# Kernel tuning notes

Measured on AMD Instinct MI355X. Metric: run time of the kernel, lower is better.

The kernel has to match this reference:

```python
import jax, jax.numpy as jnp
import numpy as np

N = 20000   # num_nodes
D = 128     # node_dim
H = 128     # hidden_dim (also per-head channels, PyG out_channels is per-head)
EV = 64     # event_dim
NH = 4      # heads
E = 250000  # num edges
NT = 8      # num_event_types
K = 4       # active event types


def setup_inputs() -> dict:
    key = jax.random.key(0)
    ks = jax.random.split(key, 24)
    def w(i, shape, s=0.05):
        return jax.random.normal(ks[i], shape, dtype=jnp.float32) * s
    z = lambda shape: jnp.zeros(shape, jnp.float32)
    o = lambda shape: jnp.ones(shape, jnp.float32)
    return {
        "node_ids": jnp.arange(N, dtype=jnp.int32),
        "event_type_ids": jax.random.randint(ks[0], (K,), 0, NT, dtype=jnp.int32),
        "src": jax.random.randint(ks[1], (E,), 0, N, dtype=jnp.int32),
        "dst": jax.random.randint(ks[2], (E,), 0, N, dtype=jnp.int32),
        "event_features": jax.random.normal(ks[3], (EV,), dtype=jnp.float32),
        "event_intensity": jax.random.uniform(ks[4], (K,), dtype=jnp.float32),
        "node_emb_table": w(5, (N, D), 1.0),
        "event_type_table": w(6, (NT, H), 0.5),
        "ev_w1": w(7, (EV, H)), "ev_b1": z((H,)), "ev_g1": o((H,)), "ev_bt1": z((H,)),
        "ev_w2": w(8, (H, H)), "ev_b2": z((H,)), "ev_g2": o((H,)), "ev_bt2": z((H,)),
        "wq": w(9, (D + H, NH * H)), "bq": z((NH * H,)),
        "wk": w(10, (D + H, NH * H)), "bk": z((NH * H,)),
        "wv": w(11, (D + H, NH * H)), "bv": z((NH * H,)),
        "wskip": w(12, (D + H, H)), "bskip": z((H,)),
        "g0_w": w(13, (H, NH * H)), "g0_as": w(14, (NH, H), 0.1), "g0_ad": w(15, (NH, H), 0.1), "g0_b": z((H,)),
        "g1_w": w(16, (H, NH * H)), "g1_as": w(17, (NH, H), 0.1), "g1_ad": w(18, (NH, H), 0.1), "g1_b": z((H,)),
        "wih": w(19, (H, 4 * H)), "whh": w(20, (H, 4 * H)), "bih": z((4 * H,)), "bhh": z((4 * H,)),
    }


def layer_norm(x, g, b, eps=1e-5):
    mu = jnp.mean(x, axis=-1, keepdims=True)
    var = jnp.mean(jnp.square(x - mu), axis=-1, keepdims=True)
    return (x - mu) * jax.lax.rsqrt(var + eps) * g + b


def segment_softmax(logits, seg, n):
    # logits: [E, NH]; softmax over edges sharing the same destination seg id
    m = jax.ops.segment_max(logits, seg, num_segments=n)
    m = jnp.where(jnp.isfinite(m), m, 0.0)  # guard empty segments
    e = jnp.exp(logits - m[seg])
    s = jax.ops.segment_sum(e, seg, num_segments=n)
    return e / (s[seg] + 1e-16)


def _forward(node_ids, event_type_ids, src, dst,
             event_features, event_intensity, node_emb_table, event_type_table,
             ev_w1, ev_b1, ev_g1, ev_bt1, ev_w2, ev_b2, ev_g2, ev_bt2,
             wq, bq, wk, bk, wv, bv, wskip, bskip,
             g0_w, g0_as, g0_ad, g0_b, g1_w, g1_as, g1_ad, g1_b,
             wih, whh, bih, bhh):
    node_emb = node_emb_table[node_ids]                                      # [N, D]
    # event encoder MLP (dropout off / eval mode)
    e = jax.nn.relu(layer_norm(event_features @ ev_w1 + ev_b1, ev_g1, ev_bt1))
    e = jax.nn.relu(layer_norm(e @ ev_w2 + ev_b2, ev_g2, ev_bt2))            # [H]
    # intensity-weighted mean of active event-type embeddings
    e = e + jnp.mean(event_type_table[event_type_ids] * event_intensity[:, None], axis=0)
    x = jnp.concatenate([node_emb, jnp.broadcast_to(e, (N, H))], axis=1)     # [N, D+H]

    # --- TransformerConv (heads=NH, concat=False -> head mean, root_weight skip) ---
    q = (x @ wq + bq).reshape(N, NH, H)
    k = (x @ wk + bk).reshape(N, NH, H)
    v = (x @ wv + bv).reshape(N, NH, H)
    alpha = jnp.sum(q[dst] * k[src], axis=-1) / jnp.sqrt(jnp.float32(H))     # [E, NH]
    alpha = segment_softmax(alpha, dst, N)
    agg = jax.ops.segment_sum(v[src] * alpha[..., None], dst, num_segments=N)  # [N, NH, H]
    x = agg.mean(axis=1) + x @ wskip + bskip                                 # [N, H]

    sl = jnp.arange(N, dtype=src.dtype)
    src2 = jnp.concatenate([src, sl])
    dst2 = jnp.concatenate([dst, sl])
    for w_, asrc, adst, b_ in ((g0_w, g0_as, g0_ad, g0_b), (g1_w, g1_as, g1_ad, g1_b)):
        xh = (x @ w_).reshape(N, NH, H)
        a_s = jnp.sum(xh * asrc, axis=-1)                                    # [N, NH]
        a_d = jnp.sum(xh * adst, axis=-1)
        ee = jax.nn.leaky_relu(a_s[src2] + a_d[dst2], 0.2)                   # [E+N, NH]
        a = segment_softmax(ee, dst2, N)
        out = jax.ops.segment_sum(xh[src2] * a[..., None], dst2, num_segments=N)
        x = jax.nn.relu(out.mean(axis=1) + b_)                               # [N, H]

    # --- batched LSTMCell, zero initial (h, c); torch gate order i, f, g, o ---
    h0 = jnp.zeros((N, H), x.dtype)
    c0 = jnp.zeros((N, H), x.dtype)
    gates = x @ wih + bih + h0 @ whh + bhh                                   # [N, 4H]
    gi, gf, gg, go = jnp.split(gates, 4, axis=-1)
    c = jax.nn.sigmoid(gf) * c0 + jax.nn.sigmoid(gi) * jnp.tanh(gg)
    h = jax.nn.sigmoid(go) * jnp.tanh(c)
    return h, c


def reference(node_ids, event_type_ids, src, dst,
              event_features, event_intensity, node_emb_table, event_type_table,
              ev_w1, ev_b1, ev_g1, ev_bt1, ev_w2, ev_b2, ev_g2, ev_bt2,
              wq, bq, wk, bk, wv, bv, wskip, bskip,
              g0_w, g0_as, g0_ad, g0_b, g1_w, g1_as, g1_ad, g1_b,
              wih, whh, bih, bhh):
    return _forward(node_ids, event_type_ids, src, dst,
                    event_features, event_intensity, node_emb_table, event_type_table,
                    ev_w1, ev_b1, ev_g1, ev_bt1, ev_w2, ev_b2, ev_g2, ev_bt2,
                    wq, bq, wk, bk, wv, bv, wskip, bskip,
                    g0_w, g0_as, g0_ad, g0_b, g1_w, g1_as, g1_ad, g1_b,
                    wih, whh, bih, bhh)
```

## Files before the change

### kernel.cpp

```cpp
#include <hip/hip_runtime.h>
#include <math.h>

#define D_DIM 128
#define H_DIM 128
#define SQRT_H_INV 0.08838834764831845f
#define BCOL_QKV 0
#define BCOL_G0 1664
#define BCOL_G1 2176
#define BCOL_W  2688
#define BCOL_TOT 3072

typedef unsigned short u16;
typedef unsigned short ushort8v __attribute__((ext_vector_type(8)));
typedef __bf16 bf16x8 __attribute__((ext_vector_type(8)));
typedef float f32x4 __attribute__((ext_vector_type(4)));


__device__ __forceinline__ float grp16_sum(float v) {
  v += __shfl_xor(v, 1);
  v += __shfl_xor(v, 2);
  v += __shfl_xor(v, 4);
  v += __shfl_xor(v, 8);
  return v;
}

__device__ __forceinline__ void split_bf16(float x, u16& h, u16& l) {
  __bf16 hb = (__bf16)x;
  float rm = x - (float)hb;
  __bf16 lb = (__bf16)rm;
  h = __builtin_bit_cast(u16, hb);
  l = __builtin_bit_cast(u16, lb);
}

__global__ __launch_bounds__(128) void k_event(
    const float* __restrict__ ef, int EV,
    const float* __restrict__ w1, const float* __restrict__ b1,
    const float* __restrict__ g1, const float* __restrict__ bt1,
    const float* __restrict__ w2, const float* __restrict__ b2,
    const float* __restrict__ g2, const float* __restrict__ bt2,
    const float* __restrict__ ett, const int* __restrict__ etid,
    const float* __restrict__ inten, int K,
    float* __restrict__ e_out)
{
  __shared__ float sh[H_DIM];
  __shared__ float red[H_DIM];
  const int t = threadIdx.x;

  float acc = b1[t];
  for (int i = 0; i < EV; ++i) acc += ef[i] * w1[i * H_DIM + t];

  red[t] = acc; __syncthreads();
  for (int s = 64; s > 0; s >>= 1) { if (t < s) red[t] += red[t + s]; __syncthreads(); }
  float mu = red[0] / H_DIM; __syncthreads();
  float d = acc - mu;
  red[t] = d * d; __syncthreads();
  for (int s = 64; s > 0; s >>= 1) { if (t < s) red[t] += red[t + s]; __syncthreads(); }
  float var = red[0] / H_DIM; __syncthreads();
  float y = d * rsqrtf(var + 1e-5f) * g1[t] + bt1[t];
  y = fmaxf(y, 0.f);
  sh[t] = y; __syncthreads();

  float acc2 = b2[t];
  for (int i = 0; i < H_DIM; ++i) acc2 += sh[i] * w2[i * H_DIM + t];

  red[t] = acc2; __syncthreads();
  for (int s = 64; s > 0; s >>= 1) { if (t < s) red[t] += red[t + s]; __syncthreads(); }
  mu = red[0] / H_DIM; __syncthreads();
  d = acc2 - mu;
  red[t] = d * d; __syncthreads();
  for (int s = 64; s > 0; s >>= 1) { if (t < s) red[t] += red[t + s]; __syncthreads(); }
  var = red[0] / H_DIM; __syncthreads();
  float y2 = d * rsqrtf(var + 1e-5f) * g2[t] + bt2[t];
  y2 = fmaxf(y2, 0.f);

  float m = 0.f;
  for (int k = 0; k < K; ++k) m += ett[etid[k] * H_DIM + t] * inten[k];
  e_out[t] = y2 + m / (float)K;
}

__global__ __launch_bounds__(256) void k_cvec_all(
    const float* __restrict__ e,
    const float* __restrict__ wq, const float* __restrict__ bq,
    const float* __restrict__ wk, const float* __restrict__ bk,
    const float* __restrict__ wv, const float* __restrict__ bv,
    const float* __restrict__ wskip, const float* __restrict__ bskip,
    const float* __restrict__ bih, const float* __restrict__ bhh,
    float* __restrict__ cvec1, float* __restrict__ cvec2)
{
  __shared__ float es[H_DIM];
  const int t = threadIdx.x;
  if (t < H_DIM) es[t] = e[t];
  __syncthreads();
  int j = blockIdx.x * 256 + t;
  if (j < 1664) {
    const float* W; const float* b; int col; int stride;
    if (j < 512)       { W = wq;    b = bq;    col = j;        stride = 512; }
    else if (j < 1024) { W = wk;    b = bk;    col = j - 512;  stride = 512; }
    else if (j < 1536) { W = wv;    b = bv;    col = j - 1024; stride = 512; }
    else               { W = wskip; b = bskip; col = j - 1536; stride = 128; }
    float a = b[col];
    for (int i = 0; i < H_DIM; ++i) a += es[i] * W[(D_DIM + i) * stride + col];
    cvec1[j] = a;
  } else if (j < 1664 + 384) {
    int j2 = j - 1664;
    int src = (j2 < 128) ? j2 : j2 + 128;
    cvec2[j2] = bih[src] + bhh[src];
  }
}

__global__ __launch_bounds__(256) void k_split_all(
    const float* __restrict__ wq, const float* __restrict__ wk,
    const float* __restrict__ wv, const float* __restrict__ wskip,
    const float* __restrict__ g0w, const float* __restrict__ g1w,
    const float* __restrict__ wih,
    u16* __restrict__ hi, u16* __restrict__ lo)
{
  int idx = blockIdx.x * 256 + threadIdx.x;
  if (idx >= BCOL_TOT * 16) return;
  int n = idx >> 4, g = idx & 15;
  const float* W; int col, stride;
  if (n < 512)        { W = wq;    col = n;        stride = 512; }
  else if (n < 1024)  { W = wk;    col = n - 512;  stride = 512; }
  else if (n < 1536)  { W = wv;    col = n - 1024; stride = 512; }
  else if (n < 1664)  { W = wskip; col = n - 1536; stride = 128; }
  else if (n < 2176)  { W = g0w;   col = n - 1664; stride = 512; }
  else if (n < 2688)  { W = g1w;   col = n - 2176; stride = 512; }
  else { int c = n - 2688; W = wih; col = (c < 128) ? c : c + 128; stride = 512; }
  size_t dst = (size_t)(n >> 4) * 2048 + g * 128 + (n & 15) * 8;
#pragma unroll
  for (int j = 0; j < 8; ++j) {
    u16 h, l;
    split_bf16(W[(size_t)(g * 8 + j) * stride + col], h, l);
    hi[dst + j] = h; lo[dst + j] = l;
  }
}

__global__ __launch_bounds__(256) void k_split_a(
    const float* __restrict__ A, const int* __restrict__ ids,
    u16* __restrict__ hi, u16* __restrict__ lo, int M, int Mpad)
{
  int idx = blockIdx.x * 256 + threadIdx.x;
  if (idx >= Mpad * 16) return;
  int row = idx >> 4, g = idx & 15;
  size_t dst = (size_t)(row >> 4) * 2048 + g * 128 + (row & 15) * 8;
  if (row < M) {
    int ar = ids ? ids[row] : row;
    const float* srcp = A + (size_t)ar * 128 + g * 8;
#pragma unroll
    for (int j = 0; j < 8; ++j) {
      u16 h, l;
      split_bf16(srcp[j], h, l);
      hi[dst + j] = h; lo[dst + j] = l;
    }
  } else {
#pragma unroll
    for (int j = 0; j < 8; ++j) { hi[dst + j] = 0; lo[dst + j] = 0; }
  }
}

__global__ __launch_bounds__(256, 3) void mfma_gemm(
    const u16* __restrict__ Ahi, const u16* __restrict__ Alo,
    const u16* __restrict__ Bhi, const u16* __restrict__ Blo,
    const float* __restrict__ cvec,
    u16* __restrict__ bf_out, int bf_cols,
    float* __restrict__ f32_out, int f32_lo, int ld_f32,
    const float* __restrict__ asw, const float* __restrict__ adw,
    float* __restrict__ a_s, float* __restrict__ a_d,
    int M)
{
  __shared__ float red[256];

  const int t = threadIdx.x;
  const int bm = blockIdx.y * 128;
  const int bn = blockIdx.x * 128;
  const int lane = t & 63;
  const int wid = t >> 6;
  const int wr = wid >> 1, wc = wid & 1;
  const int lg = lane >> 4;
  const int lr = lane & 15;

  const int arb = (bm >> 4) + wr * 4;
  const int brb = (bn >> 4) + wc * 4;

  f32x4 acc[4][4];
  const f32x4 zero = {0.f, 0.f, 0.f, 0.f};
#pragma unroll
  for (int i = 0; i < 4; ++i)
#pragma unroll
    for (int j = 0; j < 4; ++j) acc[i][j] = zero;

#pragma unroll
  for (int ks = 0; ks < 4; ++ks) {
    const int g = ks * 4 + lg;
    bf16x8 ah[4], al[4], bh[4], bl[4];
#pragma unroll
    for (int i = 0; i < 4; ++i) {
      size_t oa = (size_t)(arb + i) * 2048 + g * 128 + lr * 8;
      ah[i] = *(const bf16x8*)&Ahi[oa];
      al[i] = *(const bf16x8*)&Alo[oa];
      size_t ob = (size_t)(brb + i) * 2048 + g * 128 + lr * 8;
      bh[i] = *(const bf16x8*)&Bhi[ob];
      bl[i] = *(const bf16x8*)&Blo[ob];
    }
#pragma unroll
    for (int i = 0; i < 4; ++i)
#pragma unroll
      for (int j = 0; j < 4; ++j) {
        acc[i][j] = __builtin_amdgcn_mfma_f32_16x16x32_bf16(ah[i], bh[j], acc[i][j], 0, 0, 0);
        acc[i][j] = __builtin_amdgcn_mfma_f32_16x16x32_bf16(ah[i], bl[j], acc[i][j], 0, 0, 0);
        acc[i][j] = __builtin_amdgcn_mfma_f32_16x16x32_bf16(al[i], bh[j], acc[i][j], 0, 0, 0);
      }
  }

  const int rq = (lane >> 4) << 2;
  const int cq = lane & 15;
  const int head = bn >> 7;

  float ws_[4], wd_[4];
  if (asw) {
#pragma unroll
    for (int j = 0; j < 4; ++j) {
      int cc = (wc * 64 + j * 16 + cq) & 127;
      ws_[j] = asw[head * 128 + cc];
      wd_[j] = adw[head * 128 + cc];
    }
    if (t < 256) red[t] = 0.f;
    __syncthreads();
  }

#pragma unroll
  for (int i = 0; i < 4; ++i) {
#pragma unroll
    for (int r = 0; r < 4; ++r) {
      int rowl = wr * 64 + i * 16 + rq + r;
      int row = bm + rowl;
      bool rok = row < M;
      float ps = 0.f, pd = 0.f;
#pragma unroll
      for (int j = 0; j < 4; ++j) {
        int col = bn + wc * 64 + j * 16 + cq;
        float a = acc[i][j][r];
        if (rok) {
          float val = a + (cvec ? cvec[col] : 0.f);
          if (bf_out && col < bf_cols)
            bf_out[(size_t)row * bf_cols + col] =
                __builtin_bit_cast(u16, (__bf16)val);
          if (f32_out && col >= f32_lo)
            f32_out[(size_t)row * ld_f32 + (col - f32_lo)] = val;
        }
        if (asw) { ps += a * ws_[j]; pd += a * wd_[j]; }
      }
      if (asw && rok) {
        atomicAdd(&red[rowl], ps);
        atomicAdd(&red[128 + rowl], pd);
      }
    }
  }
  if (asw) {
    __syncthreads();
    if (t < 128) {
      int row = bm + t;
      if (row < M) {
        a_s[row * 4 + head] = red[t];
        a_d[row * 4 + head] = red[128 + t];
      }
    }
  }
}

__global__ __launch_bounds__(256) void k_zero(int* __restrict__ p, int n) {
  int i = blockIdx.x * 256 + threadIdx.x;
  if (i < n) p[i] = 0;
}
__global__ __launch_bounds__(256) void k_count(
    const int* __restrict__ dst, int* __restrict__ counts, int E) {
  int e = blockIdx.x * 256 + threadIdx.x;
  if (e < E) atomicAdd(&counts[dst[e]], 1);
}
__global__ __launch_bounds__(1024) void k_scan(
    const int* __restrict__ counts, int* __restrict__ offs,
    int* __restrict__ cursor, int N)
{
  __shared__ int wsum[16];
  const int t = threadIdx.x;
  const int lane = t & 63;
  const int wid = t >> 6;
  int running = 0;
  for (int base = 0; base < N; base += 1024) {
    int v = (base + t < N) ? counts[base + t] : 0;
    int incl = v;
#pragma unroll
    for (int s = 1; s < 64; s <<= 1) {
      int u = __shfl_up(incl, s);
      if (lane >= s) incl += u;
    }
    if (lane == 63) wsum[wid] = incl;
    __syncthreads();
    if (wid == 0) {
      int w = (lane < 16) ? wsum[lane] : 0;
#pragma unroll
      for (int s = 1; s < 16; s <<= 1) {
        int u = __shfl_up(w, s);
        if (lane >= s) w += u;
      }
      if (lane < 16) wsum[lane] = w;
    }
    __syncthreads();
    int wpre = (wid > 0) ? wsum[wid - 1] : 0;
    int tot = wsum[15];
    int inclg = incl + wpre;
    if (base + t < N) {
      offs[base + t + 1] = running + inclg;
      cursor[base + t] = running + inclg - v;
    }
    running += tot;
    __syncthreads();
  }
  if (t == 0) offs[0] = 0;
}
__global__ __launch_bounds__(256) void k_fill(
    const int* __restrict__ src, const int* __restrict__ dst,
    int* __restrict__ cursor, int* __restrict__ csr_src, int E) {
  int e = blockIdx.x * 256 + threadIdx.x;
  if (e < E) {
    int slot = atomicAdd(&cursor[dst[e]], 1);
    csr_src[slot] = src[e];
  }
}

__global__ __launch_bounds__(256) void k_tconv(
    const u16* __restrict__ QKVp, const float* __restrict__ skipbuf,
    const int* __restrict__ offs, const int* __restrict__ csr_src,
    u16* __restrict__ Xhi, u16* __restrict__ Xlo, int N)
{
  const int wid = threadIdx.x >> 6;
  const int lane = threadIdx.x & 63;
  const int node = blockIdx.x * 4 + wid;
  if (node >= N) {
    if (lane < 16) {
      size_t dst = (size_t)(node >> 4) * 2048 + lane * 128 + (node & 15) * 8;
#pragma unroll
      for (int j = 0; j < 8; ++j) { Xhi[dst + j] = 0; Xlo[dst + j] = 0; }
    }
    return;
  }
  float q[8];
  {
    bf16x8 qv = *(const bf16x8*)(QKVp + (size_t)node * 1536 + lane * 8);
#pragma unroll
    for (int j = 0; j < 8; ++j) q[j] = (float)qv[j];
  }
  const int beg = offs[node], end = offs[node + 1];
  float mx = -1e30f;
  float ssum = 0.f;
  float acc[8] = {0.f,0.f,0.f,0.f,0.f,0.f,0.f,0.f};

  int e = beg;
  for (; e + 4 <= end; e += 4) {
    int s0 = csr_src[e];
    int s1 = csr_src[e + 1];
    int s2 = csr_src[e + 2];
    int s3 = csr_src[e + 3];
    const u16* r0 = QKVp + (size_t)s0 * 1536 + 512 + lane * 8;
    const u16* r1 = QKVp + (size_t)s1 * 1536 + 512 + lane * 8;
    const u16* r2 = QKVp + (size_t)s2 * 1536 + 512 + lane * 8;
    const u16* r3 = QKVp + (size_t)s3 * 1536 + 512 + lane * 8;
    bf16x8 k0 = *(const bf16x8*)(r0);
    bf16x8 k1 = *(const bf16x8*)(r1);
    bf16x8 k2 = *(const bf16x8*)(r2);
    bf16x8 k3 = *(const bf16x8*)(r3);
    bf16x8 v0 = *(const bf16x8*)(r0 + 512);
    bf16x8 v1 = *(const bf16x8*)(r1 + 512);
    bf16x8 v2 = *(const bf16x8*)(r2 + 512);
    bf16x8 v3 = *(const bf16x8*)(r3 + 512);
    float p0 = 0.f, p1 = 0.f, p2 = 0.f, p3 = 0.f;
#pragma unroll
    for (int j = 0; j < 8; ++j) {
      p0 += q[j] * (float)k0[j];
      p1 += q[j] * (float)k1[j];
      p2 += q[j] * (float)k2[j];
      p3 += q[j] * (float)k3[j];
    }
    p0 = grp16_sum(p0) * SQRT_H_INV;
    p1 = grp16_sum(p1) * SQRT_H_INV;
    p2 = grp16_sum(p2) * SQRT_H_INV;
    p3 = grp16_sum(p3) * SQRT_H_INV;
    float nm = fmaxf(fmaxf(fmaxf(p0, p1), fmaxf(p2, p3)), mx);
    float sc = expf(mx - nm);
    float w0 = expf(p0 - nm);
    float w1 = expf(p1 - nm);
    float w2 = expf(p2 - nm);
    float w3 = expf(p3 - nm);
    ssum = ssum * sc + (w0 + w1) + (w2 + w3);
#pragma unroll
    for (int j = 0; j < 8; ++j)
      acc[j] = acc[j] * sc + (w0 * (float)v0[j] + w1 * (float)v1[j])
                           + (w2 * (float)v2[j] + w3 * (float)v3[j]);
    mx = nm;
  }
  for (; e < end; ++e) {
    int s0 = csr_src[e];
    const u16* r0 = QKVp + (size_t)s0 * 1536 + 512 + lane * 8;
    bf16x8 ka = *(const bf16x8*)(r0);
    bf16x8 va = *(const bf16x8*)(r0 + 512);
    float p0 = 0.f;
#pragma unroll
    for (int j = 0; j < 8; ++j) p0 += q[j] * (float)ka[j];
    p0 = grp16_sum(p0) * SQRT_H_INV;
    float nm = fmaxf(mx, p0);
    float sc = expf(mx - nm);
    float w0 = expf(p0 - nm);
    ssum = ssum * sc + w0;
#pragma unroll
    for (int j = 0; j < 8; ++j)
      acc[j] = acc[j] * sc + w0 * (float)va[j];
    mx = nm;
  }

  float inv = 1.f / (ssum + 1e-16f);
#pragma unroll
  for (int j = 0; j < 8; ++j) acc[j] *= inv;
#pragma unroll
  for (int j = 0; j < 8; ++j) {
    acc[j] += __shfl_xor(acc[j], 16);
    acc[j] += __shfl_xor(acc[j], 32);
  }
  if (lane < 16) {
    const float* sk = skipbuf + (size_t)node * 128 + lane * 8;
    size_t dst = (size_t)(node >> 4) * 2048 + lane * 128 + (node & 15) * 8;
#pragma unroll
    for (int j = 0; j < 8; ++j) {
      float x = 0.25f * acc[j] + sk[j];
      u16 h, l;
      split_bf16(x, h, l);
      Xhi[dst + j] = h; Xlo[dst + j] = l;
    }
  }
}

__global__ __launch_bounds__(256) void k_gat_agg(
    const u16* __restrict__ xhb,
    const float* __restrict__ a_s, const float* __restrict__ a_d,
    const int* __restrict__ offs, const int* __restrict__ csr_src,
    const float* __restrict__ bias,
    u16* __restrict__ Xhi, u16* __restrict__ Xlo, int N)
{
  const int wid = threadIdx.x >> 6;
  const int lane = threadIdx.x & 63;
  const int node = blockIdx.x * 4 + wid;
  if (node >= N) {
    if (lane < 16) {
      size_t dst = (size_t)(node >> 4) * 2048 + lane * 128 + (node & 15) * 8;
#pragma unroll
      for (int j = 0; j < 8; ++j) { Xhi[dst + j] = 0; Xlo[dst + j] = 0; }
    }
    return;
  }
  const int head = lane >> 4;
  const float adn = a_d[node * 4 + head];
  const float asn = a_s[node * 4 + head];
  float lself = asn + adn;
  lself = lself >= 0.f ? lself : 0.2f * lself;

  float mx = lself;
  float ssum = 1.f;
  float acc[8];
  {
    bf16x8 xs = *(const bf16x8*)(xhb + (size_t)node * 512 + lane * 8);
#pragma unroll
    for (int j = 0; j < 8; ++j) acc[j] = (float)xs[j];
  }

  const int beg = offs[node], end = offs[node + 1];
  int e = beg;
  for (; e + 4 <= end; e += 4) {
    int s0 = csr_src[e];
    int s1 = csr_src[e + 1];
    int s2 = csr_src[e + 2];
    int s3 = csr_src[e + 3];
    float l0 = a_s[s0 * 4 + head];
    float l1 = a_s[s1 * 4 + head];
    float l2 = a_s[s2 * 4 + head];
    float l3 = a_s[s3 * 4 + head];
    const u16* r0 = xhb + (size_t)s0 * 512 + lane * 8;
    const u16* r1 = xhb + (size_t)s1 * 512 + lane * 8;
    const u16* r2 = xhb + (size_t)s2 * 512 + lane * 8;
    const u16* r3 = xhb + (size_t)s3 * 512 + lane * 8;
    bf16x8 xa = *(const bf16x8*)(r0);
    bf16x8 xb = *(const bf16x8*)(r1);
    bf16x8 xc = *(const bf16x8*)(r2);
    bf16x8 xd = *(const bf16x8*)(r3);
    l0 += adn; l1 += adn; l2 += adn; l3 += adn;
    l0 = l0 >= 0.f ? l0 : 0.2f * l0;
    l1 = l1 >= 0.f ? l1 : 0.2f * l1;
    l2 = l2 >= 0.f ? l2 : 0.2f * l2;
    l3 = l3 >= 0.f ? l3 : 0.2f * l3;
    float nm = fmaxf(fmaxf(fmaxf(l0, l1), fmaxf(l2, l3)), mx);
    float sc = expf(mx - nm);
    float w0 = expf(l0 - nm);
    float w1 = expf(l1 - nm);
    float w2 = expf(l2 - nm);
    float w3 = expf(l3 - nm);
    ssum = ssum * sc + (w0 + w1) + (w2 + w3);
#pragma unroll
    for (int j = 0; j < 8; ++j)
      acc[j] = acc[j] * sc + (w0 * (float)xa[j] + w1 * (float)xb[j])
                           + (w2 * (float)xc[j] + w3 * (float)xd[j]);
    mx = nm;
  }
  for (; e < end; ++e) {
    int s0 = csr_src[e];
    float l0 = a_s[s0 * 4 + head] + adn;
    l0 = l0 >= 0.f ? l0 : 0.2f * l0;
    const u16* r0 = xhb + (size_t)s0 * 512 + lane * 8;
    bf16x8 xa = *(const bf16x8*)(r0);
    float nm = fmaxf(mx, l0);
    float sc = expf(mx - nm);
    float w0 = expf(l0 - nm);
    ssum = ssum * sc + w0;
#pragma unroll
    for (int j = 0; j < 8; ++j)
      acc[j] = acc[j] * sc + w0 * (float)xa[j];
    mx = nm;
  }

  float inv = 1.f / (ssum + 1e-16f);
#pragma unroll
  for (int j = 0; j < 8; ++j) acc[j] *= inv;
#pragma unroll
  for (int j = 0; j < 8; ++j) {
    acc[j] += __shfl_xor(acc[j], 16);
    acc[j] += __shfl_xor(acc[j], 32);
  }
  if (lane < 16) {
    const float* b = bias + lane * 8;
    size_t dst = (size_t)(node >> 4) * 2048 + lane * 128 + (node & 15) * 8;
#pragma unroll
    for (int j = 0; j < 8; ++j) {
      float x = fmaxf(0.25f * acc[j] + b[j], 0.f);
      u16 h, l;
      split_bf16(x, h, l);
      Xhi[dst + j] = h; Xlo[dst + j] = l;
    }
  }
}

__global__ __launch_bounds__(256) void k_lstm(
    const float* __restrict__ gates, float* __restrict__ out, int N)
{
  int idx = blockIdx.x * 256 + threadIdx.x;
  if (idx >= N * 128) return;
  int n = idx >> 7, c = idx & 127;
  const float* g = gates + (size_t)n * 384;
  float gi = g[c], gg = g[128 + c], go = g[256 + c];
  float cv = (1.f / (1.f + expf(-gi))) * tanhf(gg);
  float hv = (1.f / (1.f + expf(-go))) * tanhf(cv);
  out[idx] = hv;
  out[(size_t)N * 128 + idx] = cv;
}

extern "C" void kernel_launch(void* const* d_in, const int* in_sizes, int n_in,
                              void* d_out, int out_size, void* d_ws, size_t ws_size,
                              hipStream_t stream) {
  const int*   node_ids = (const int*)d_in[0];
  const int*   etid     = (const int*)d_in[1];
  const int*   src      = (const int*)d_in[2];
  const int*   dst      = (const int*)d_in[3];
  const float* ef       = (const float*)d_in[4];
  const float* inten    = (const float*)d_in[5];
  const float* nemb     = (const float*)d_in[6];
  const float* ett      = (const float*)d_in[7];
  const float* ev_w1 = (const float*)d_in[8],  *ev_b1 = (const float*)d_in[9];
  const float* ev_g1 = (const float*)d_in[10], *ev_bt1 = (const float*)d_in[11];
  const float* ev_w2 = (const float*)d_in[12], *ev_b2 = (const float*)d_in[13];
  const float* ev_g2 = (const float*)d_in[14], *ev_bt2 = (const float*)d_in[15];
  const float* wq = (const float*)d_in[16], *bq = (const float*)d_in[17];
  const float* wk = (const float*)d_in[18], *bk = (const float*)d_in[19];
  const float* wv = (const float*)d_in[20], *bv = (const float*)d_in[21];
  const float* wskip = (const float*)d_in[22], *bskip = (const float*)d_in[23];
  const float* g0_w = (const float*)d_in[24], *g0_as = (const float*)d_in[25];
  const float* g0_ad = (const float*)d_in[26], *g0_b = (const float*)d_in[27];
  const float* g1_w = (const float*)d_in[28], *g1_as = (const float*)d_in[29];
  const float* g1_ad = (const float*)d_in[30], *g1_b = (const float*)d_in[31];
  const float* wih = (const float*)d_in[32];
  const float* bih = (const float*)d_in[34], *bhh = (const float*)d_in[35];

  const int N = in_sizes[0];
  const int K = in_sizes[1];
  const int E = in_sizes[2];
  const int EV = in_sizes[4];

  const int gridMy = (N + 127) / 128;
  const int Npad = gridMy * 128;

  float* ws = (float*)d_ws;
  size_t o = 0;
  float* e_vec = ws + o; o += 128;
  float* cvec1 = ws + o; o += 1664;
  float* cvec2 = ws + o; o += 384;
  u16* Ballhi = (u16*)(ws + o); o += (size_t)BCOL_TOT * 64;
  u16* Balllo = (u16*)(ws + o); o += (size_t)BCOL_TOT * 64;
  u16* Ahi  = (u16*)(ws + o); o += (size_t)Npad * 64;
  u16* Alo  = (u16*)(ws + o); o += (size_t)Npad * 64;
  u16* XShi = (u16*)(ws + o); o += (size_t)Npad * 64;
  u16* XSlo = (u16*)(ws + o); o += (size_t)Npad * 64;
  u16* QKVp = (u16*)(ws + o); o += (size_t)Npad * 768;
  float* skipbuf = ws + o; o += (size_t)Npad * 128;
  u16* xhb  = (u16*)(ws + o); o += (size_t)Npad * 256;
  float* gates = ws + o; o += (size_t)Npad * 192;
  float* a_s   = ws + o; o += (size_t)N * 4;
  float* a_d   = ws + o; o += (size_t)N * 4;
  int* counts  = (int*)(ws + o); o += N;
  int* offs    = (int*)(ws + o); o += (size_t)N + 1;
  int* cursor  = (int*)(ws + o); o += N;
  int* csr_src = (int*)(ws + o); o += E;

  float* out = (float*)d_out;
  const int nodeBlocksPad = Npad / 4;

  k_event<<<1, 128, 0, stream>>>(ef, EV, ev_w1, ev_b1, ev_g1, ev_bt1,
                                 ev_w2, ev_b2, ev_g2, ev_bt2,
                                 ett, etid, inten, K, e_vec);
  k_cvec_all<<<8, 256, 0, stream>>>(e_vec, wq, bq, wk, bk, wv, bv,
                                    wskip, bskip, bih, bhh, cvec1, cvec2);
  k_split_all<<<(BCOL_TOT * 16) / 256, 256, 0, stream>>>(
      wq, wk, wv, wskip, g0_w, g1_w, wih, Ballhi, Balllo);
  k_split_a<<<(Npad * 16 + 255) / 256, 256, 0, stream>>>(nemb, node_ids, Ahi, Alo, N, Npad);

  k_zero<<<(N + 255) / 256, 256, 0, stream>>>(counts, N);
  k_count<<<(E + 255) / 256, 256, 0, stream>>>(dst, counts, E);
  k_scan<<<1, 1024, 0, stream>>>(counts, offs, cursor, N);
  k_fill<<<(E + 255) / 256, 256, 0, stream>>>(src, dst, cursor, csr_src, E);

  mfma_gemm<<<dim3(13, gridMy), 256, 0, stream>>>(
      Ahi, Alo, Ballhi + (size_t)BCOL_QKV * 128, Balllo + (size_t)BCOL_QKV * 128,
      cvec1, QKVp, 1536, skipbuf, 1536, 128,
      nullptr, nullptr, nullptr, nullptr, N);

  k_tconv<<<nodeBlocksPad, 256, 0, stream>>>(QKVp, skipbuf, offs, csr_src,
                                             XShi, XSlo, N);

  mfma_gemm<<<dim3(4, gridMy), 256, 0, stream>>>(
      XShi, XSlo, Ballhi + (size_t)BCOL_G0 * 128, Balllo + (size_t)BCOL_G0 * 128,
      nullptr, xhb, 512, nullptr, 0, 0,
      g0_as, g0_ad, a_s, a_d, N);
  k_gat_agg<<<nodeBlocksPad, 256, 0, stream>>>(xhb, a_s, a_d, offs, csr_src,
                                               g0_b, XShi, XSlo, N);

  mfma_gemm<<<dim3(4, gridMy), 256, 0, stream>>>(
      XShi, XSlo, Ballhi + (size_t)BCOL_G1 * 128, Balllo + (size_t)BCOL_G1 * 128,
      nullptr, xhb, 512, nullptr, 0, 0,
      g1_as, g1_ad, a_s, a_d, N);
  k_gat_agg<<<nodeBlocksPad, 256, 0, stream>>>(xhb, a_s, a_d, offs, csr_src,
                                               g1_b, XShi, XSlo, N);

  mfma_gemm<<<dim3(3, gridMy), 256, 0, stream>>>(
      XShi, XSlo, Ballhi + (size_t)BCOL_W * 128, Balllo + (size_t)BCOL_W * 128,
      cvec2, nullptr, 0, gates, 0, 384,
      nullptr, nullptr, nullptr, nullptr, N);
  k_lstm<<<((N * 128) + 255) / 256, 256, 0, stream>>>(gates, out, N);
}
```

Baseline: 453.9 us.

## Use bf16 dot2, packed f32x2 math and lazy max rescale in attention aggregation

Rewrites the per-edge online-softmax loops in the transformer conv and GAT kernels. QK dot products now use v_dot2_f32_bf16 inline asm on packed bf16 pairs. V accumulation uses f32x2 vectors with bit-shift bf16-to-float conversion so the compiler can emit packed FMA. The running-max rescale is skipped when no lane sees a new max. Together these cut per-edge ALU work, in exchange for inline asm dependence and a wave-uniform branch.

```diff
diff --git a/kernel.cpp b/kernel.cpp
--- a/kernel.cpp
+++ b/kernel.cpp
@@ -11,9 +11,12 @@
 #define BCOL_TOT 3072
 
 typedef unsigned short u16;
+typedef unsigned int u32;
 typedef unsigned short ushort8v __attribute__((ext_vector_type(8)));
+typedef unsigned int u32x4 __attribute__((ext_vector_type(4)));
 typedef __bf16 bf16x8 __attribute__((ext_vector_type(8)));
 typedef float f32x4 __attribute__((ext_vector_type(4)));
+typedef float f32x2 __attribute__((ext_vector_type(2)));
 
 
 __device__ __forceinline__ float grp16_sum(float v) {
@@ -30,6 +33,22 @@
   __bf16 lb = (__bf16)rm;
   h = __builtin_bit_cast(u16, hb);
   l = __builtin_bit_cast(u16, lb);
+}
+
+__device__ __forceinline__ f32x2 cvt2(u32 v) {
+  f32x2 r;
+  r[0] = __builtin_bit_cast(float, v << 16);
+  r[1] = __builtin_bit_cast(float, v & 0xffff0000u);
+  return r;
+}
+
+__device__ __forceinline__ float qk_dot(const u32x4 q, const u32x4 k) {
+  float p = 0.f;
+  asm("v_dot2_f32_bf16 %0, %1, %2, %0" : "+v"(p) : "v"(q[0]), "v"(k[0]));
+  asm("v_dot2_f32_bf16 %0, %1, %2, %0" : "+v"(p) : "v"(q[1]), "v"(k[1]));
+  asm("v_dot2_f32_bf16 %0, %1, %2, %0" : "+v"(p) : "v"(q[2]), "v"(k[2]));
+  asm("v_dot2_f32_bf16 %0, %1, %2, %0" : "+v"(p) : "v"(q[3]), "v"(k[3]));
+  return p;
 }
 
 __global__ __launch_bounds__(128) void k_event(
@@ -344,16 +363,14 @@
     }
     return;
   }
-  float q[8];
-  {
-    bf16x8 qv = *(const bf16x8*)(QKVp + (size_t)node * 1536 + lane * 8);
-#pragma unroll
-    for (int j = 0; j < 8; ++j) q[j] = (float)qv[j];
-  }
+  const u32x4 q = *(const u32x4*)(QKVp + (size_t)node * 1536 + lane * 8);
+
   const int beg = offs[node], end = offs[node + 1];
   float mx = -1e30f;
   float ssum = 0.f;
-  float acc[8] = {0.f,0.f,0.f,0.f,0.f,0.f,0.f,0.f};
+  f32x2 acc2[4];
+#pragma unroll
+  for (int jj = 0; jj < 4; ++jj) acc2[jj] = (f32x2){0.f, 0.f};
 
   int e = beg;
   for (; e + 4 <= end; e += 4) {
@@ -365,61 +382,74 @@
     const u16* r1 = QKVp + (size_t)s1 * 1536 + 512 + lane * 8;
     const u16* r2 = QKVp + (size_t)s2 * 1536 + 512 + lane * 8;
     const u16* r3 = QKVp + (size_t)s3 * 1536 + 512 + lane * 8;
-    bf16x8 k0 = *(const bf16x8*)(r0);
-    bf16x8 k1 = *(const bf16x8*)(r1);
-    bf16x8 k2 = *(const bf16x8*)(r2);
-    bf16x8 k3 = *(const bf16x8*)(r3);
-    bf16x8 v0 = *(const bf16x8*)(r0 + 512);
-    bf16x8 v1 = *(const bf16x8*)(r1 + 512);
-    bf16x8 v2 = *(const bf16x8*)(r2 + 512);
-    bf16x8 v3 = *(const bf16x8*)(r3 + 512);
-    float p0 = 0.f, p1 = 0.f, p2 = 0.f, p3 = 0.f;
-#pragma unroll
-    for (int j = 0; j < 8; ++j) {
-      p0 += q[j] * (float)k0[j];
-      p1 += q[j] * (float)k1[j];
-      p2 += q[j] * (float)k2[j];
-      p3 += q[j] * (float)k3[j];
-    }
+    u32x4 k0 = *(const u32x4*)(r0);
+    u32x4 k1 = *(const u32x4*)(r1);
+    u32x4 k2 = *(const u32x4*)(r2);
+    u32x4 k3 = *(const u32x4*)(r3);
+    u32x4 v0 = *(const u32x4*)(r0 + 512);
+    u32x4 v1 = *(const u32x4*)(r1 + 512);
+    u32x4 v2 = *(const u32x4*)(r2 + 512);
+    u32x4 v3 = *(const u32x4*)(r3 + 512);
+    float p0 = qk_dot(q, k0);
+    float p1 = qk_dot(q, k1);
+    float p2 = qk_dot(q, k2);
+    float p3 = qk_dot(q, k3);
     p0 = grp16_sum(p0) * SQRT_H_INV;
     p1 = grp16_sum(p1) * SQRT_H_INV;
     p2 = grp16_sum(p2) * SQRT_H_INV;
     p3 = grp16_sum(p3) * SQRT_H_INV;
-    float nm = fmaxf(fmaxf(fmaxf(p0, p1), fmaxf(p2, p3)), mx);
-    float sc = expf(mx - nm);
-    float w0 = expf(p0 - nm);
-    float w1 = expf(p1 - nm);
-    float w2 = expf(p2 - nm);
-    float w3 = expf(p3 - nm);
-    ssum = ssum * sc + (w0 + w1) + (w2 + w3);
-#pragma unroll
-    for (int j = 0; j < 8; ++j)
-      acc[j] = acc[j] * sc + (w0 * (float)v0[j] + w1 * (float)v1[j])
-                           + (w2 * (float)v2[j] + w3 * (float)v3[j]);
-    mx = nm;
+    float pmax = fmaxf(fmaxf(p0, p1), fmaxf(p2, p3));
+    if (!__all(pmax <= mx)) {
+      float nm = fmaxf(mx, pmax);
+      float sc = expf(mx - nm);
+      f32x2 sc2 = {sc, sc};
+      ssum *= sc;
+#pragma unroll
+      for (int jj = 0; jj < 4; ++jj) acc2[jj] *= sc2;
+      mx = nm;
+    }
+    float w0 = expf(p0 - mx);
+    float w1 = expf(p1 - mx);
+    float w2 = expf(p2 - mx);
+    float w3 = expf(p3 - mx);
+    ssum += (w0 + w1) + (w2 + w3);
+    f32x2 w02 = {w0, w0}, w12 = {w1, w1}, w22 = {w2, w2}, w32 = {w3, w3};
+#pragma unroll
+    for (int jj = 0; jj < 4; ++jj)
+      acc2[jj] = acc2[jj] + (w02 * cvt2(v0[jj]) + w12 * cvt2(v1[jj]))
+                          + (w22 * cvt2(v2[jj]) + w32 * cvt2(v3[jj]));
   }
   for (; e < end; ++e) {
     int s0 = csr_src[e];
     const u16* r0 = QKVp + (size_t)s0 * 1536 + 512 + lane * 8;
-    bf16x8 ka = *(const bf16x8*)(r0);
-    bf16x8 va = *(const bf16x8*)(r0 + 512);
-    float p0 = 0.f;
-#pragma unroll
-    for (int j = 0; j < 8; ++j) p0 += q[j] * (float)ka[j];
+    u32x4 k0 = *(const u32x4*)(r0);
+    u32x4 v0 = *(const u32x4*)(r0 + 512);
+    float p0 = qk_dot(q, k0);
     p0 = grp16_sum(p0) * SQRT_H_INV;
-    float nm = fmaxf(mx, p0);
-    float sc = expf(mx - nm);
-    float w0 = expf(p0 - nm);
-    ssum = ssum * sc + w0;
-#pragma unroll
-    for (int j = 0; j < 8; ++j)
-      acc[j] = acc[j] * sc + w0 * (float)va[j];
-    mx = nm;
+    if (!__all(p0 <= mx)) {
+      float nm = fmaxf(mx, p0);
+      float sc = expf(mx - nm);
+      f32x2 sc2 = {sc, sc};
+      ssum *= sc;
+#pragma unroll
+      for (int jj = 0; jj < 4; ++jj) acc2[jj] *= sc2;
+      mx = nm;
+    }
+    float w0 = expf(p0 - mx);
+    ssum += w0;
+    f32x2 w02 = {w0, w0};
+#pragma unroll
+    for (int jj = 0; jj < 4; ++jj)
+      acc2[jj] = acc2[jj] + w02 * cvt2(v0[jj]);
   }
 
   float inv = 1.f / (ssum + 1e-16f);
-#pragma unroll
-  for (int j = 0; j < 8; ++j) acc[j] *= inv;
+  float acc[8];
+#pragma unroll
+  for (int jj = 0; jj < 4; ++jj) {
+    acc[jj * 2]     = acc2[jj][0] * inv;
+    acc[jj * 2 + 1] = acc2[jj][1] * inv;
+  }
 #pragma unroll
   for (int j = 0; j < 8; ++j) {
     acc[j] += __shfl_xor(acc[j], 16);
@@ -464,11 +494,11 @@
 
   float mx = lself;
   float ssum = 1.f;
-  float acc[8];
+  f32x2 acc2[4];
   {
-    bf16x8 xs = *(const bf16x8*)(xhb + (size_t)node * 512 + lane * 8);
-#pragma unroll
-    for (int j = 0; j < 8; ++j) acc[j] = (float)xs[j];
+    u32x4 xs = *(const u32x4*)(xhb + (size_t)node * 512 + lane * 8);
+#pragma unroll
+    for (int jj = 0; jj < 4; ++jj) acc2[jj] = cvt2(xs[jj]);
   }
 
   const int beg = offs[node], end = offs[node + 1];
@@ -486,47 +516,66 @@
     const u16* r1 = xhb + (size_t)s1 * 512 + lane * 8;
     const u16* r2 = xhb + (size_t)s2 * 512 + lane * 8;
     const u16* r3 = xhb + (size_t)s3 * 512 + lane * 8;
-    bf16x8 xa = *(const bf16x8*)(r0);
-    bf16x8 xb = *(const bf16x8*)(r1);
-    bf16x8 xc = *(const bf16x8*)(r2);
-    bf16x8 xd = *(const bf16x8*)(r3);
+    u32x4 xa = *(const u32x4*)(r0);
+    u32x4 xb = *(const u32x4*)(r1);
+    u32x4 xc = *(const u32x4*)(r2);
+    u32x4 xd = *(const u32x4*)(r3);
     l0 += adn; l1 += adn; l2 += adn; l3 += adn;
     l0 = l0 >= 0.f ? l0 : 0.2f * l0;
     l1 = l1 >= 0.f ? l1 : 0.2f * l1;
     l2 = l2 >= 0.f ? l2 : 0.2f * l2;
     l3 = l3 >= 0.f ? l3 : 0.2f * l3;
-    float nm = fmaxf(fmaxf(fmaxf(l0, l1), fmaxf(l2, l3)), mx);
-    float sc = expf(mx - nm);
-    float w0 = expf(l0 - nm);
-    float w1 = expf(l1 - nm);
-    float w2 = expf(l2 - nm);
-    float w3 = expf(l3 - nm);
-    ssum = ssum * sc + (w0 + w1) + (w2 + w3);
-#pragma unroll
-    for (int j = 0; j < 8; ++j)
-      acc[j] = acc[j] * sc + (w0 * (float)xa[j] + w1 * (float)xb[j])
-                           + (w2 * (float)xc[j] + w3 * (float)xd[j]);
-    mx = nm;
+    float lmax = fmaxf(fmaxf(l0, l1), fmaxf(l2, l3));
+    if (!__all(lmax <= mx)) {
+      float nm = fmaxf(mx, lmax);
+      float sc = expf(mx - nm);
+      f32x2 sc2 = {sc, sc};
+      ssum *= sc;
+#pragma unroll
+      for (int jj = 0; jj < 4; ++jj) acc2[jj] *= sc2;
+      mx = nm;
+    }
+    float w0 = expf(l0 - mx);
+    float w1 = expf(l1 - mx);
+    float w2 = expf(l2 - mx);
+    float w3 = expf(l3 - mx);
+    ssum += (w0 + w1) + (w2 + w3);
+    f32x2 w02 = {w0, w0}, w12 = {w1, w1}, w22 = {w2, w2}, w32 = {w3, w3};
+#pragma unroll
+    for (int jj = 0; jj < 4; ++jj)
+      acc2[jj] = acc2[jj] + (w02 * cvt2(xa[jj]) + w12 * cvt2(xb[jj]))
+                          + (w22 * cvt2(xc[jj]) + w32 * cvt2(xd[jj]));
   }
   for (; e < end; ++e) {
     int s0 = csr_src[e];
     float l0 = a_s[s0 * 4 + head] + adn;
     l0 = l0 >= 0.f ? l0 : 0.2f * l0;
     const u16* r0 = xhb + (size_t)s0 * 512 + lane * 8;
-    bf16x8 xa = *(const bf16x8*)(r0);
-    float nm = fmaxf(mx, l0);
-    float sc = expf(mx - nm);
-    float w0 = expf(l0 - nm);
-    ssum = ssum * sc + w0;
-#pragma unroll
-    for (int j = 0; j < 8; ++j)
-      acc[j] = acc[j] * sc + w0 * (float)xa[j];
-    mx = nm;
+    u32x4 xa = *(const u32x4*)(r0);
+    if (!__all(l0 <= mx)) {
+      float nm = fmaxf(mx, l0);
+      float sc = expf(mx - nm);
+      f32x2 sc2 = {sc, sc};
+      ssum *= sc;
+#pragma unroll
+      for (int jj = 0; jj < 4; ++jj) acc2[jj] *= sc2;
+      mx = nm;
+    }
+    float w0 = expf(l0 - mx);
+    ssum += w0;
+    f32x2 w02 = {w0, w0};
+#pragma unroll
+    for (int jj = 0; jj < 4; ++jj)
+      acc2[jj] = acc2[jj] + w02 * cvt2(xa[jj]);
   }
 
   float inv = 1.f / (ssum + 1e-16f);
-#pragma unroll
-  for (int j = 0; j < 8; ++j) acc[j] *= inv;
+  float acc[8];
+#pragma unroll
+  for (int jj = 0; jj < 4; ++jj) {
+    acc[jj * 2]     = acc2[jj][0] * inv;
+    acc[jj * 2 + 1] = acc2[jj][1] * inv;
+  }
 #pragma unroll
   for (int j = 0; j < 8; ++j) {
     acc[j] += __shfl_xor(acc[j], 16);
```

New measurement: 461.2 us. No clear change (+1.6%).
